# Performance work log

Measured on AMD Instinct MI355X. Metric: run time of the kernel, lower is better.

Reference implementation:

```python
import jax, jax.numpy as jnp
import numpy as np


def _proj(W, b, x):
    # 1x1 conv == per-pixel GEMM over channels: [O,C] x [B,C,H,W] -> [B,O,H,W]
    return jnp.einsum('oc,bchw->bohw', W, x) + b[None, :, None, None]


def _cross(src, ctx, Wq, bq, Wk, bk, Wv, bv):
    # queries from src, keys/values from ctx; returns [B,C,H,W]
    B, C, H, W = src.shape
    HW = H * W
    q = _proj(Wq, bq, src).reshape(B, -1, HW)   # [B, C//8, HW]
    k = _proj(Wk, bk, ctx).reshape(B, -1, HW)   # [B, C//8, HW]
    v = _proj(Wv, bv, ctx).reshape(B, C, HW)    # [B, C,    HW]
    # attn[b,i,j] = softmax_j( q[b,:,i] . k[b,:,j] )
    attn = jax.nn.softmax(jnp.einsum('bci,bcj->bij', q, k), axis=-1)
    out = jnp.einsum('bcj,bij->bci', v, attn)   # [B, C, HW]
    return out.reshape(B, C, H, W)


def setup_inputs() -> dict:
    key = jax.random.key(0)
    ks = jax.random.split(key, 8)
    dim = 256
    B, H, W = 4, 64, 64
    return {
        'x': jax.random.normal(ks[0], (B, dim, H, W), jnp.float32),
        'y': jax.random.normal(ks[1], (B, dim, H, W), jnp.float32),
        'Wq': jax.random.normal(ks[2], (dim // 8, dim), jnp.float32) * 0.05,
        'bq': jax.random.normal(ks[3], (dim // 8,), jnp.float32) * 0.05,
        'Wk': jax.random.normal(ks[4], (dim // 8, dim), jnp.float32) * 0.05,
        'bk': jax.random.normal(ks[5], (dim // 8,), jnp.float32) * 0.05,
        'Wv': jax.random.normal(ks[6], (dim, dim), jnp.float32) * 0.05,
        'bv': jax.random.normal(ks[7], (dim,), jnp.float32) * 0.05,
    }


def reference(x, y, Wq, bq, Wk, bk, Wv, bv):
    outx = _cross(x, y, Wq, bq, Wk, bk, Wv, bv)  # x queries attend to y
    outy = _cross(y, x, Wq, bq, Wk, bk, Wv, bv)  # y queries attend to x
    return (outx, outy)
```

## Files before the change

kernel.cpp:

```cpp
#include <hip/hip_runtime.h>

#define BB 4
#define CC 256
#define DD 32
#define SS 4096

typedef __bf16 bf16;
typedef __bf16 bf16x8 __attribute__((ext_vector_type(8)));
typedef __bf16 bf16x4 __attribute__((ext_vector_type(4)));
typedef float f32x4 __attribute__((ext_vector_type(4)));
typedef unsigned int u32;
typedef unsigned short u16;

#define Q_OFF  0
#define K_OFF  1048576
#define V_OFF  2097152
#define WB_OFF 10485760

static __device__ __forceinline__ u32 pack2(float lo, float hi) {
    bf16 a = (bf16)lo, b = (bf16)hi;
    u16 ua = __builtin_bit_cast(u16, a), ub = __builtin_bit_cast(u16, b);
    return (u32)ua | ((u32)ub << 16);
}

static __device__ __forceinline__ void bar_lds() {
    asm volatile("s_waitcnt lgkmcnt(0)" ::: "memory");
    __builtin_amdgcn_s_barrier();
    asm volatile("" ::: "memory");
}

__global__ __launch_bounds__(256) void convert_w_kernel(
    const float* __restrict__ Wq, const float* __restrict__ Wk,
    const float* __restrict__ Wv, bf16* __restrict__ wb)
{
    const int gid = blockIdx.x*256 + threadIdx.x;
    const int idx = gid*8;
    const int o = idx >> 8, cc = idx & 255;
    const float* row = (o < 32) ? (Wq + (size_t)o*CC)
                     : (o < 64) ? (Wk + (size_t)(o-32)*CC)
                                : (Wv + (size_t)(o-64)*CC);
    const float4 a = *(const float4*)(row + cc);
    const float4 c = *(const float4*)(row + cc + 4);
    bf16x8 pk;
    pk[0]=(bf16)a.x; pk[1]=(bf16)a.y; pk[2]=(bf16)a.z; pk[3]=(bf16)a.w;
    pk[4]=(bf16)c.x; pk[5]=(bf16)c.y; pk[6]=(bf16)c.z; pk[7]=(bf16)c.w;
    *(bf16x8*)(wb + idx) = pk;
}

__global__ __launch_bounds__(256, 2) void proj_all_kernel(
    const float* __restrict__ x, const float* __restrict__ y,
    const bf16* __restrict__ wb,
    const float* __restrict__ bq, const float* __restrict__ bk,
    const float* __restrict__ bv,
    bf16* __restrict__ qout, bf16* __restrict__ kout, bf16* __restrict__ vout)
{
    __shared__ __align__(16) char smem[2*5120];
    bf16* xT  = (bf16*)smem;
    u32*  xTw = (u32*)smem;

    const int t    = threadIdx.x;
    const int lane = t & 63;
    const int w    = t >> 6;
    const int ln   = lane & 15;
    const int quad = lane >> 4;

    const int bid  = blockIdx.x;
    const int dirb = bid & 7;
    const int src  = dirb >> 2;
    const int b    = dirb & 3;
    const int i0   = (bid >> 3) * 64;
    const float* in = src ? y : x;
    const float* xbase = in + (size_t)b*CC*SS + i0;

    const int cp = t >> 4;
    const int pq = (t & 15) * 4;

    float bias[5];
    #pragma unroll
    for (int nbl = 0; nbl < 5; ++nbl) {
        const int o = 80*w + nbl*16 + ln;
        bias[nbl] = (o < 32) ? bq[o] : (o < 64) ? bk[o-32] : bv[o-64];
    }
    f32x4 acc[4][5];
    #pragma unroll
    for (int mb = 0; mb < 4; ++mb)
        #pragma unroll
        for (int nbl = 0; nbl < 5; ++nbl)
            acc[mb][nbl] = (f32x4){bias[nbl], bias[nbl], bias[nbl], bias[nbl]};

    const bf16* wrow = wb + (size_t)(80*w + ln)*CC + quad*8;
    bf16x8 bf[5];
    #pragma unroll
    for (int nbl = 0; nbl < 5; ++nbl)
        bf[nbl] = *(const bf16x8*)(wrow + (size_t)nbl*16*CC);

    {
        const float* r0 = xbase + (size_t)(2*cp)*SS + pq;
        const float4 a0 = *(const float4*)r0;
        const float4 a1 = *(const float4*)(r0 + SS);
        xTw[(pq+0)*20 + cp] = pack2(a0.x, a1.x);
        xTw[(pq+1)*20 + cp] = pack2(a0.y, a1.y);
        xTw[(pq+2)*20 + cp] = pack2(a0.z, a1.z);
        xTw[(pq+3)*20 + cp] = pack2(a0.w, a1.w);
    }
    float4 a0, a1;
    {
        const float* r1 = xbase + (size_t)(32 + 2*cp)*SS + pq;
        a0 = *(const float4*)r1;
        a1 = *(const float4*)(r1 + SS);
    }
    bar_lds();

    for (int n = 0; n < 8; ++n) {
        bf16x8 af[4];
        #pragma unroll
        for (int mb = 0; mb < 4; ++mb)
            af[mb] = *(const bf16x8*)(xT + (n&1)*2560 + (mb*16 + ln)*40 + quad*8);
        if (n < 7) {
            u32* dst = xTw + ((n+1)&1)*1280;
            dst[(pq+0)*20 + cp] = pack2(a0.x, a1.x);
            dst[(pq+1)*20 + cp] = pack2(a0.y, a1.y);
            dst[(pq+2)*20 + cp] = pack2(a0.z, a1.z);
            dst[(pq+3)*20 + cp] = pack2(a0.w, a1.w);
        }
        {
            const int cc2 = ((n+2)*32) & 255;
            const float* r2 = xbase + (size_t)(cc2 + 2*cp)*SS + pq;
            a0 = *(const float4*)r2;
            a1 = *(const float4*)(r2 + SS);
        }
        #pragma unroll
        for (int mb = 0; mb < 4; ++mb)
            #pragma unroll
            for (int nbl = 0; nbl < 5; ++nbl)
                acc[mb][nbl] = __builtin_amdgcn_mfma_f32_16x16x32_bf16(
                                   af[mb], bf[nbl], acc[mb][nbl], 0, 0, 0);
        const int ccn = ((n+1)*32) & 255;
        #pragma unroll
        for (int nbl = 0; nbl < 5; ++nbl)
            bf[nbl] = *(const bf16x8*)(wrow + (size_t)nbl*16*CC + ccn);
        bar_lds();
    }

    bf16* qo = qout + (size_t)(src*BB + b)*SS*DD;
    bf16* ko = kout + (size_t)(src*BB + b)*SS*DD;
    bf16* vo = vout + (size_t)(src*BB + b)*CC*SS;
    #pragma unroll
    for (int nbl = 0; nbl < 5; ++nbl) {
        const int o = 80*w + nbl*16 + ln;
        if (o < 32) {
            #pragma unroll
            for (int mb = 0; mb < 4; ++mb)
                #pragma unroll
                for (int r = 0; r < 4; ++r)
                    qo[(size_t)(i0 + mb*16 + quad*4 + r)*DD + o] = (bf16)acc[mb][nbl][r];
        } else if (o < 64) {
            #pragma unroll
            for (int mb = 0; mb < 4; ++mb)
                #pragma unroll
                for (int r = 0; r < 4; ++r)
                    ko[(size_t)(i0 + mb*16 + quad*4 + r)*DD + (o-32)] = (bf16)acc[mb][nbl][r];
        } else {
            const int c = o - 64;
            #pragma unroll
            for (int mb = 0; mb < 4; ++mb) {
                bf16x4 pk;
                #pragma unroll
                for (int r = 0; r < 4; ++r) pk[r] = (bf16)acc[mb][nbl][r];
                *(bf16x4*)(vo + (size_t)c*SS + i0 + mb*16 + quad*4) = pk;
            }
        }
    }
}

#define SM_M 16.0f

__global__ __launch_bounds__(256, 2) void attn_kernel(
    const bf16* __restrict__ qg, const bf16* __restrict__ kg,
    const bf16* __restrict__ vg, float* __restrict__ out)
{
    __shared__ __align__(16) char smem[16640];
    bf16*  p_s = (bf16*)smem;
    float* l_s = (float*)(smem + 16384);

    const int t    = threadIdx.x;
    const int lane = t & 63;
    const int w    = t >> 6;
    const int ln   = lane & 15;
    const int quad = lane >> 4;

    const int bid  = blockIdx.x;
    const int dirb = bid & 7;
    const int dir  = dirb >> 2;
    const int b    = dirb & 3;
    const int i0   = (bid >> 3) * 64;

    const bf16* q = qg + ((size_t)dir*BB + b)*SS*DD + (size_t)i0*DD;
    const bf16* k = kg + ((size_t)(1-dir)*BB + b)*SS*DD;
    const bf16* v = vg + ((size_t)(1-dir)*BB + b)*CC*SS;
    float* op = out + ((size_t)dir*BB + b)*CC*SS;

    const bf16x8 b_q = *(const bf16x8*)(q + (size_t)(w*16 + ln)*DD + quad*8);
    const bf16* kbase = k + (size_t)ln*DD + quad*8;
    const bf16* vptr[4];
    #pragma unroll
    for (int cb = 0; cb < 4; ++cb)
        vptr[cb] = v + (size_t)(w*64 + cb*16 + ln)*SS + quad*8;

    f32x4 o[4][4];
    #pragma unroll
    for (int qb = 0; qb < 4; ++qb)
        #pragma unroll
        for (int cb = 0; cb < 4; ++cb) o[qb][cb] = (f32x4){0.f,0.f,0.f,0.f};
    f32x4 lpv = (f32x4){0.f,0.f,0.f,0.f};

    const int swz  = ln & 7;
    const int prow = (w*16 + ln)*64;

    bf16x8 kfA[4], kfB[4], vfA[2][4], vfB[2][4];
    {
        bf16x8 k0[4];
        #pragma unroll
        for (int nb = 0; nb < 4; ++nb)
            k0[nb]  = *(const bf16x8*)(kbase + (size_t)(nb*16)*DD);
        #pragma unroll
        for (int nb = 0; nb < 4; ++nb)
            kfB[nb] = *(const bf16x8*)(kbase + (size_t)(64  + nb*16)*DD);
        #pragma unroll
        for (int nb = 0; nb < 4; ++nb)
            kfA[nb] = *(const bf16x8*)(kbase + (size_t)(128 + nb*16)*DD);
        #pragma unroll
        for (int ks = 0; ks < 2; ++ks)
            #pragma unroll
            for (int cb = 0; cb < 4; ++cb) {
                vfA[ks][cb] = *(const bf16x8*)(vptr[cb] + ks*32);
                vfB[ks][cb] = *(const bf16x8*)(vptr[cb] + 64 + ks*32);
            }
        f32x4 s[4];
        #pragma unroll
        for (int nb = 0; nb < 4; ++nb)
            s[nb] = __builtin_amdgcn_mfma_f32_16x16x32_bf16(
                        k0[nb], b_q, (f32x4){0.f,0.f,0.f,0.f}, 0, 0, 0);
        #pragma unroll
        for (int nb = 0; nb < 4; ++nb) {
            bf16x4 pk;
            #pragma unroll
            for (int r = 0; r < 4; ++r) {
                const float e = __expf(fminf(s[nb][r] - SM_M, 60.0f));
                lpv[r] += e;
                pk[r] = (bf16)e;
            }
            *(bf16x4*)(p_s + prow + (((2*nb + (quad >> 1)) ^ swz) << 3)
                       + (quad & 1)*4) = pk;
        }
    }

    auto attn_iter = [&](int n, bf16x8 (&vfc)[2][4], bf16x8 (&kfu)[4],
                         const bf16* pr, bf16* pw) {
        bar_lds();
        f32x4 s[4];
        if (n < 63) {
            #pragma unroll
            for (int nb = 0; nb < 4; ++nb)
                s[nb] = __builtin_amdgcn_mfma_f32_16x16x32_bf16(
                            kfu[nb], b_q, (f32x4){0.f,0.f,0.f,0.f}, 0, 0, 0);
            const int j3 = ((n + 3) << 6) & (SS - 1);
            #pragma unroll
            for (int nb = 0; nb < 4; ++nb)
                kfu[nb] = *(const bf16x8*)(kbase + (size_t)(j3 + nb*16)*DD);
        }
        #pragma unroll
        for (int ks = 0; ks < 2; ++ks) {
            bf16x8 ap[4];
            #pragma unroll
            for (int qb = 0; qb < 4; ++qb)
                ap[qb] = *(const bf16x8*)(pr + (qb*16 + ln)*64
                                          + (((ks*4 + quad) ^ swz) << 3));
            #pragma unroll
            for (int qb = 0; qb < 4; ++qb)
                #pragma unroll
                for (int cb = 0; cb < 4; ++cb)
                    o[qb][cb] = __builtin_amdgcn_mfma_f32_16x16x32_bf16(
                                    ap[qb], vfc[ks][cb], o[qb][cb], 0, 0, 0);
        }
        const int j2 = ((n + 2) << 6) & (SS - 1);
        #pragma unroll
        for (int ks = 0; ks < 2; ++ks)
            #pragma unroll
            for (int cb = 0; cb < 4; ++cb)
                vfc[ks][cb] = *(const bf16x8*)(vptr[cb] + j2 + ks*32);
        if (n < 63) {
            #pragma unroll
            for (int nb = 0; nb < 4; ++nb) {
                bf16x4 pk;
                #pragma unroll
                for (int r = 0; r < 4; ++r) {
                    const float e = __expf(fminf(s[nb][r] - SM_M, 60.0f));
                    lpv[r] += e;
                    pk[r] = (bf16)e;
                }
                *(bf16x4*)(pw + prow + (((2*nb + (quad >> 1)) ^ swz) << 3)
                           + (quad & 1)*4) = pk;
            }
        }
    };

    for (int n = 0; n < 64; n += 2) {
        attn_iter(n,     vfA, kfB, p_s,        p_s + 4096);
        attn_iter(n + 1, vfB, kfA, p_s + 4096, p_s);
    }

    float lp = (lpv[0] + lpv[1]) + (lpv[2] + lpv[3]);
    lp += __shfl_xor(lp, 16);
    lp += __shfl_xor(lp, 32);
    if (lane < 16) l_s[w*16 + ln] = lp;
    __syncthreads();

    #pragma unroll
    for (int qb = 0; qb < 4; ++qb) {
        const f32x4 lq = *(const f32x4*)(l_s + qb*16 + quad*4);
        const float ri0 = 1.0f/lq[0], ri1 = 1.0f/lq[1], ri2 = 1.0f/lq[2], ri3 = 1.0f/lq[3];
        #pragma unroll
        for (int cb = 0; cb < 4; ++cb) {
            const int c = w*64 + cb*16 + ln;
            float4 val = make_float4(o[qb][cb][0]*ri0, o[qb][cb][1]*ri1,
                                     o[qb][cb][2]*ri2, o[qb][cb][3]*ri3);
            *(float4*)(op + (size_t)c*SS + i0 + qb*16 + quad*4) = val;
        }
    }
}

extern "C" void kernel_launch(void* const* d_in, const int* in_sizes, int n_in,
                              void* d_out, int out_size, void* d_ws, size_t ws_size,
                              hipStream_t stream)
{
    const float* x  = (const float*)d_in[0];
    const float* y  = (const float*)d_in[1];
    const float* Wq = (const float*)d_in[2];
    const float* bq = (const float*)d_in[3];
    const float* Wk = (const float*)d_in[4];
    const float* bk = (const float*)d_in[5];
    const float* Wv = (const float*)d_in[6];
    const float* bv = (const float*)d_in[7];
    float* out = (float*)d_out;
    bf16* ws   = (bf16*)d_ws;

    bf16* qw = ws + Q_OFF;
    bf16* kw = ws + K_OFF;
    bf16* vw = ws + V_OFF;
    bf16* wb = ws + WB_OFF;

    convert_w_kernel<<<40,  256, 0, stream>>>(Wq, Wk, Wv, wb);
    proj_all_kernel <<<512, 256, 0, stream>>>(x, y, wb, bq, bk, bv, qw, kw, vw);
    attn_kernel     <<<512, 256, 0, stream>>>(qw, kw, vw, out);
}
```

Baseline: 255.4 us.

## Split attention channels across two blocks to double grid and raise occupancy

The attention kernel now splits the 256 output channels into two halves, one per block, so the grid grows from 512 to 1024 blocks. Each wave keeps fewer accumulators and V fragments, and launch bounds rise to 4 blocks per CU. Prefetch depth drops from two tiles ahead to one, the exp moves to exp2 with a folded constant, and s_setprio raises priority around the PV MFMAs. The cost is that each half recomputes QK^T and the softmax numerators, so that work is duplicated, and the shallower prefetch may expose more load latency.

```diff
diff --git a/kernel.cpp b/kernel.cpp
--- a/kernel.cpp
+++ b/kernel.cpp
@@ -173,9 +173,11 @@
     }
 }
 
-#define SM_M 16.0f
-
-__global__ __launch_bounds__(256, 2) void attn_kernel(
+#define SM_M  16.0f
+#define L2E   1.4426950408889634f
+#define SM_C  (SM_M * L2E)
+
+__global__ __launch_bounds__(256, 4) void attn_kernel(
     const bf16* __restrict__ qg, const bf16* __restrict__ kg,
     const bf16* __restrict__ vg, float* __restrict__ out)
 {
@@ -193,7 +195,8 @@
     const int dirb = bid & 7;
     const int dir  = dirb >> 2;
     const int b    = dirb & 3;
-    const int i0   = (bid >> 3) * 64;
+    const int c0   = ((bid >> 3) & 1) * 128;
+    const int i0   = (bid >> 4) * 64;
 
     const bf16* q = qg + ((size_t)dir*BB + b)*SS*DD + (size_t)i0*DD;
     const bf16* k = kg + ((size_t)(1-dir)*BB + b)*SS*DD;
@@ -202,51 +205,45 @@
 
     const bf16x8 b_q = *(const bf16x8*)(q + (size_t)(w*16 + ln)*DD + quad*8);
     const bf16* kbase = k + (size_t)ln*DD + quad*8;
-    const bf16* vptr[4];
-    #pragma unroll
-    for (int cb = 0; cb < 4; ++cb)
-        vptr[cb] = v + (size_t)(w*64 + cb*16 + ln)*SS + quad*8;
-
-    f32x4 o[4][4];
+    const bf16* vptr[2];
+    #pragma unroll
+    for (int cb = 0; cb < 2; ++cb)
+        vptr[cb] = v + (size_t)(c0 + w*32 + cb*16 + ln)*SS + quad*8;
+
+    f32x4 o[4][2];
     #pragma unroll
     for (int qb = 0; qb < 4; ++qb)
         #pragma unroll
-        for (int cb = 0; cb < 4; ++cb) o[qb][cb] = (f32x4){0.f,0.f,0.f,0.f};
+        for (int cb = 0; cb < 2; ++cb) o[qb][cb] = (f32x4){0.f,0.f,0.f,0.f};
     f32x4 lpv = (f32x4){0.f,0.f,0.f,0.f};
 
     const int swz  = ln & 7;
     const int prow = (w*16 + ln)*64;
 
-    bf16x8 kfA[4], kfB[4], vfA[2][4], vfB[2][4];
+    bf16x8 kf[4], vf[2][2];
     {
-        bf16x8 k0[4];
         #pragma unroll
         for (int nb = 0; nb < 4; ++nb)
-            k0[nb]  = *(const bf16x8*)(kbase + (size_t)(nb*16)*DD);
-        #pragma unroll
-        for (int nb = 0; nb < 4; ++nb)
-            kfB[nb] = *(const bf16x8*)(kbase + (size_t)(64  + nb*16)*DD);
-        #pragma unroll
-        for (int nb = 0; nb < 4; ++nb)
-            kfA[nb] = *(const bf16x8*)(kbase + (size_t)(128 + nb*16)*DD);
+            kf[nb] = *(const bf16x8*)(kbase + (size_t)(nb*16)*DD);
         #pragma unroll
         for (int ks = 0; ks < 2; ++ks)
             #pragma unroll
-            for (int cb = 0; cb < 4; ++cb) {
-                vfA[ks][cb] = *(const bf16x8*)(vptr[cb] + ks*32);
-                vfB[ks][cb] = *(const bf16x8*)(vptr[cb] + 64 + ks*32);
-            }
+            for (int cb = 0; cb < 2; ++cb)
+                vf[ks][cb] = *(const bf16x8*)(vptr[cb] + ks*32);
         f32x4 s[4];
         #pragma unroll
         for (int nb = 0; nb < 4; ++nb)
             s[nb] = __builtin_amdgcn_mfma_f32_16x16x32_bf16(
-                        k0[nb], b_q, (f32x4){0.f,0.f,0.f,0.f}, 0, 0, 0);
+                        kf[nb], b_q, (f32x4){0.f,0.f,0.f,0.f}, 0, 0, 0);
+        #pragma unroll
+        for (int nb = 0; nb < 4; ++nb)
+            kf[nb] = *(const bf16x8*)(kbase + (size_t)(64 + nb*16)*DD);
         #pragma unroll
         for (int nb = 0; nb < 4; ++nb) {
             bf16x4 pk;
             #pragma unroll
             for (int r = 0; r < 4; ++r) {
-                const float e = __expf(fminf(s[nb][r] - SM_M, 60.0f));
+                const float e = exp2f(s[nb][r]*L2E - SM_C);
                 lpv[r] += e;
                 pk[r] = (bf16)e;
             }
@@ -255,20 +252,24 @@
         }
     }
 
-    auto attn_iter = [&](int n, bf16x8 (&vfc)[2][4], bf16x8 (&kfu)[4],
-                         const bf16* pr, bf16* pw) {
+    for (int n = 0; n < 64; ++n) {
         bar_lds();
+        const bf16* pr = p_s + (n & 1)*4096;
+        bf16* pw = p_s + ((n + 1) & 1)*4096;
+
         f32x4 s[4];
         if (n < 63) {
             #pragma unroll
             for (int nb = 0; nb < 4; ++nb)
                 s[nb] = __builtin_amdgcn_mfma_f32_16x16x32_bf16(
-                            kfu[nb], b_q, (f32x4){0.f,0.f,0.f,0.f}, 0, 0, 0);
-            const int j3 = ((n + 3) << 6) & (SS - 1);
+                            kf[nb], b_q, (f32x4){0.f,0.f,0.f,0.f}, 0, 0, 0);
+            const int j2 = ((n + 2) << 6) & (SS - 1);
             #pragma unroll
             for (int nb = 0; nb < 4; ++nb)
-                kfu[nb] = *(const bf16x8*)(kbase + (size_t)(j3 + nb*16)*DD);
-        }
+                kf[nb] = *(const bf16x8*)(kbase + (size_t)(j2 + nb*16)*DD);
+        }
+
+        __builtin_amdgcn_s_setprio(1);
         #pragma unroll
         for (int ks = 0; ks < 2; ++ks) {
             bf16x8 ap[4];
@@ -279,23 +280,26 @@
             #pragma unroll
             for (int qb = 0; qb < 4; ++qb)
                 #pragma unroll
-                for (int cb = 0; cb < 4; ++cb)
+                for (int cb = 0; cb < 2; ++cb)
                     o[qb][cb] = __builtin_amdgcn_mfma_f32_16x16x32_bf16(
-                                    ap[qb], vfc[ks][cb], o[qb][cb], 0, 0, 0);
-        }
-        const int j2 = ((n + 2) << 6) & (SS - 1);
+                                    ap[qb], vf[ks][cb], o[qb][cb], 0, 0, 0);
+        }
+        __builtin_amdgcn_s_setprio(0);
+
+        const int j1 = ((n + 1) << 6) & (SS - 1);
         #pragma unroll
         for (int ks = 0; ks < 2; ++ks)
             #pragma unroll
-            for (int cb = 0; cb < 4; ++cb)
-                vfc[ks][cb] = *(const bf16x8*)(vptr[cb] + j2 + ks*32);
+            for (int cb = 0; cb < 2; ++cb)
+                vf[ks][cb] = *(const bf16x8*)(vptr[cb] + j1 + ks*32);
+
         if (n < 63) {
             #pragma unroll
             for (int nb = 0; nb < 4; ++nb) {
                 bf16x4 pk;
                 #pragma unroll
                 for (int r = 0; r < 4; ++r) {
-                    const float e = __expf(fminf(s[nb][r] - SM_M, 60.0f));
+                    const float e = exp2f(s[nb][r]*L2E - SM_C);
                     lpv[r] += e;
                     pk[r] = (bf16)e;
                 }
@@ -303,11 +307,6 @@
                            + (quad & 1)*4) = pk;
             }
         }
-    };
-
-    for (int n = 0; n < 64; n += 2) {
-        attn_iter(n,     vfA, kfB, p_s,        p_s + 4096);
-        attn_iter(n + 1, vfB, kfA, p_s + 4096, p_s);
     }
 
     float lp = (lpv[0] + lpv[1]) + (lpv[2] + lpv[3]);
@@ -321,8 +320,8 @@
         const f32x4 lq = *(const f32x4*)(l_s + qb*16 + quad*4);
         const float ri0 = 1.0f/lq[0], ri1 = 1.0f/lq[1], ri2 = 1.0f/lq[2], ri3 = 1.0f/lq[3];
         #pragma unroll
-        for (int cb = 0; cb < 4; ++cb) {
-            const int c = w*64 + cb*16 + ln;
+        for (int cb = 0; cb < 2; ++cb) {
+            const int c = c0 + w*32 + cb*16 + ln;
             float4 val = make_float4(o[qb][cb][0]*ri0, o[qb][cb][1]*ri1,
                                      o[qb][cb][2]*ri2, o[qb][cb][3]*ri3);
             *(float4*)(op + (size_t)c*SS + i0 + qb*16 + quad*4) = val;
@@ -350,7 +349,7 @@
     bf16* vw = ws + V_OFF;
     bf16* wb = ws + WB_OFF;
 
-    convert_w_kernel<<<40,  256, 0, stream>>>(Wq, Wk, Wv, wb);
-    proj_all_kernel <<<512, 256, 0, stream>>>(x, y, wb, bq, bk, bv, qw, kw, vw);
-    attn_kernel     <<<512, 256, 0, stream>>>(qw, kw, vw, out);
-}
+    convert_w_kernel<<<40,   256, 0, stream>>>(Wq, Wk, Wv, wb);
+    proj_all_kernel <<<512,  256, 0, stream>>>(x, y, wb, bq, bk, bv, qw, kw, vw);
+    attn_kernel     <<<1024, 256, 0, stream>>>(qw, kw, vw, out);
+}
```

After: 283.7 us. 1.11x slower.
